# Kernel tuning notes

Hardware: AMD Instinct MI355X
Metric: run time of the kernel (lower is better)

The kernel has to match this reference:

```python
import jax, jax.numpy as jnp
import numpy as np

N_NODES = 100000
NINP = 128
N_EDGES = 1600000
EPS = 1e-12


def _gcn_conv(x, W, b, src, dst, deg_inv_sqrt):
    # PyG GCNConv: h = x W; out = D^{-1/2}(A+I)D^{-1/2} h + b
    h = x @ W  # [N, out_dim]
    norm = deg_inv_sqrt[src] * deg_inv_sqrt[dst]  # [E]
    agg = jax.ops.segment_sum(h[src] * norm[:, None], dst, num_segments=N_NODES)
    # self-loop contribution: weight deg_inv_sqrt[i]^2
    agg = agg + h * (deg_inv_sqrt ** 2)[:, None]
    return agg + b


def setup_inputs() -> dict:
    key = jax.random.key(0)
    k1, k2, k3, k4 = jax.random.split(key, 4)
    edge_index = jax.random.randint(k1, (2, N_EDGES), 0, N_NODES, dtype=jnp.int64)
    # embedding table (xavier-normal-like), padding_idx=0 row zeroed
    emb = jax.random.normal(k2, (N_NODES, NINP), dtype=jnp.float32) * (2.0 / (N_NODES + NINP)) ** 0.5
    emb = emb.at[0].set(0.0)
    W1 = jax.random.normal(k3, (NINP, 2 * NINP), dtype=jnp.float32) * (1.0 / NINP) ** 0.5
    b1 = jnp.zeros((2 * NINP,), dtype=jnp.float32)
    W2 = jax.random.normal(k4, (2 * NINP, NINP), dtype=jnp.float32) * (1.0 / (2 * NINP)) ** 0.5
    b2 = jnp.zeros((NINP,), dtype=jnp.float32)
    return {"emb": emb, "W1": W1, "b1": b1, "W2": W2, "b2": b2, "edge_index": edge_index}


def reference(emb, W1, b1, W2, b2, edge_index):
    src, dst = edge_index[0], edge_index[1]
    # symmetric GCN degree with self-loops (in-degree on dst + 1)
    deg = jax.ops.segment_sum(jnp.ones_like(dst, dtype=emb.dtype), dst, num_segments=N_NODES) + 1.0
    deg_inv_sqrt = jax.lax.rsqrt(deg)
    x = _gcn_conv(emb, W1, b1, src, dst, deg_inv_sqrt)  # [N, 2*ninp]
    # F.normalize(p=2, dim=-1)
    x = x / jnp.maximum(jnp.linalg.norm(x, axis=-1, keepdims=True), EPS)
    # dropout in eval mode (identity)
    out = _gcn_conv(x, W2, b2, src, dst, deg_inv_sqrt)  # [N, ninp]
    return out
```

## Files before the change

kernel.cpp:

```cpp
#include <hip/hip_runtime.h>
#include <hip/hip_bf16.h>

typedef __attribute__((ext_vector_type(8))) short bf16x8;
typedef __attribute__((ext_vector_type(4))) float f32x4;

#define NBUCK 391
#define BCAP 8192


__device__ __forceinline__ ushort f2bf(float f) {
    unsigned int b = __float_as_uint(f);
    unsigned int r = (b + 0x7fffu + ((b >> 16) & 1u)) >> 16;
    return (ushort)r;
}
__device__ __forceinline__ float bflo(uint v) { return __uint_as_float(v << 16); }
__device__ __forceinline__ float bfhi(uint v) { return __uint_as_float(v & 0xffff0000u); }


__global__ __launch_bounds__(256) void prep_kernel(const float* __restrict__ W1, ushort* __restrict__ W1t,
                                                   const float* __restrict__ W2, ushort* __restrict__ W2t,
                                                   int* __restrict__ gcur) {
    int b = blockIdx.x, t = threadIdx.x;
    if (b == 0) {
        if (t < NBUCK) gcur[t] = 0;
        if (t + 256 < NBUCK) gcur[t + 256] = 0;
    } else if (b <= 128) {
        int i = (b - 1) * 256 + t;
        int n = i >> 7, k = i & 127;
        W1t[i] = f2bf(W1[(size_t)k * 256 + n]);
    } else {
        int i = (b - 129) * 256 + t;
        int n = i >> 8, k = i & 255;
        W2t[i] = f2bf(W2[(size_t)k * 128 + n]);
    }
}


__global__ __launch_bounds__(256) void bucket_kernel(const int* __restrict__ src, const int* __restrict__ dst,
                                                     int* __restrict__ gcur, int2* __restrict__ pairs,
                                                     int E, int chunk) {
    __shared__ int lcnt[NBUCK];
    for (int t = threadIdx.x; t < NBUCK; t += 256) lcnt[t] = 0;
    __syncthreads();
    int e0 = blockIdx.x * chunk;
    int e1 = e0 + chunk; if (e1 > E) e1 = E;
    for (int e = e0 + (int)threadIdx.x; e < e1; e += 256)
        atomicAdd(&lcnt[dst[e] >> 8], 1);
    __syncthreads();
    for (int t = threadIdx.x; t < NBUCK; t += 256) {
        int c = lcnt[t];
        lcnt[t] = c ? atomicAdd(&gcur[t], c) : 0;
    }
    __syncthreads();
    for (int e = e0 + (int)threadIdx.x; e < e1; e += 256) {
        int d = dst[e], s = src[e];
        int b = d >> 8;
        int p = atomicAdd(&lcnt[b], 1);
        if (p < BCAP) pairs[(size_t)b * BCAP + p] = make_int2(d, s);
    }
}


__global__ __launch_bounds__(512) void scan_buckets(const int* __restrict__ gcur, int* __restrict__ bbase,
                                                    int* __restrict__ offs, int Nn, int E) {
    int i = threadIdx.x;
    int v = (i < NBUCK) ? min(gcur[i], BCAP) : 0;
    int lane = i & 63, wid = i >> 6;
    int x = v;
#pragma unroll
    for (int d = 1; d < 64; d <<= 1) {
        int y = __shfl_up(x, d, 64);
        if (lane >= d) x += y;
    }
    __shared__ int wsum[8], wpre[8];
    if (lane == 63) wsum[wid] = x;
    __syncthreads();
    if (i == 0) {
        int run = 0;
        for (int w = 0; w < 8; ++w) { wpre[w] = run; run += wsum[w]; }
        offs[Nn] = E;
    }
    __syncthreads();
    if (i < NBUCK) bbase[i] = x - v + wpre[wid];
}


__global__ __launch_bounds__(256) void csr_kernel(const int2* __restrict__ pairs, const int* __restrict__ gcur,
                                                  const int* __restrict__ bbase,
                                                  int* __restrict__ offs, float* __restrict__ dis,
                                                  int* __restrict__ csr, int Nn) {
    int b = blockIdx.x;
    int n0 = b << 8;
    int ne = min(gcur[b], BCAP);
    __shared__ int cnt[256], off[256], pos[256];
    int i = threadIdx.x;
    cnt[i] = 0;
    __syncthreads();
    const int2* pp = pairs + (size_t)b * BCAP;
    for (int e = i; e < ne; e += 256)
        atomicAdd(&cnt[pp[e].x - n0], 1);
    __syncthreads();
    int lane = i & 63, wid = i >> 6;
    int v = cnt[i];
    int x = v;
#pragma unroll
    for (int d = 1; d < 64; d <<= 1) {
        int y = __shfl_up(x, d, 64);
        if (lane >= d) x += y;
    }
    __shared__ int wsum[4], wpre[4];
    if (lane == 63) wsum[wid] = x;
    __syncthreads();
    if (i == 0) {
        int run = 0;
        for (int w = 0; w < 4; ++w) { wpre[w] = run; run += wsum[w]; }
    }
    __syncthreads();
    int excl = x - v + wpre[wid];
    off[i] = excl;
    pos[i] = 0;
    int n = n0 + i;
    if (n < Nn) {
        offs[n] = bbase[b] + excl;
        dis[n] = rsqrtf((float)v + 1.0f);
    }
    __syncthreads();
    int base = bbase[b];
    for (int e = i; e < ne; e += 256) {
        int2 r = pp[e];
        int li = r.x - n0;
        int p = atomicAdd(&pos[li], 1);
        csr[base + off[li] + p] = r.y;
    }
}


__global__ void cast_scale_kernel(const float4* __restrict__ in, const float* __restrict__ dis,
                                  ushort4* __restrict__ out, int n4) {
    int stride = gridDim.x * blockDim.x;
    for (int i = blockIdx.x * blockDim.x + threadIdx.x; i < n4; i += stride) {
        float s = dis[i >> 5];
        float4 v = in[i];
        ushort4 o;
        o.x = f2bf(v.x * s); o.y = f2bf(v.y * s); o.z = f2bf(v.z * s); o.w = f2bf(v.w * s);
        out[i] = o;
    }
}


template <bool BIAS, bool BF16OUT>
__global__ __launch_bounds__(256) void agg_kernel(const uint* __restrict__ tbl,
                                                  const int* __restrict__ offs,
                                                  const int* __restrict__ rec,
                                                  const float* __restrict__ dis,
                                                  const float* __restrict__ bias,
                                                  void* __restrict__ outp, int Nn) {
    int gw = (int)((blockIdx.x * 256 + threadIdx.x) >> 6);
    uint lane = threadIdx.x & 63;
    if (gw >= Nn) return;
    float dn = dis[gw];
    int e0 = offs[gw], e1 = offs[gw + 1];
    uint hv = tbl[(uint)gw * 64u + lane];
    float ax = bflo(hv), ay = bfhi(hv);

    for (int base = e0; base < e1; base += 16) {
        int ee = base + (int)(lane & 15u);
        uint rr = (uint)rec[ee < e1 ? ee : e1 - 1];
        uint vv[16];
#pragma unroll
        for (int j = 0; j < 16; ++j) {
            uint idx = (uint)__shfl((int)rr, j, 64);
            vv[j] = tbl[idx * 64u + lane];
        }
#pragma unroll
        for (int j = 0; j < 16; ++j) {
            uint v = (base + j < e1) ? vv[j] : 0u;
            ax += bflo(v);
            ay += bfhi(v);
        }
    }

    ax *= dn; ay *= dn;
    if (BIAS) {
        float2 bv = reinterpret_cast<const float2*>(bias)[lane];
        ax += bv.x; ay += bv.y;
    }
    if (BF16OUT) {
        reinterpret_cast<uint*>(outp)[(uint)gw * 64u + lane] =
            (uint)f2bf(ax) | ((uint)f2bf(ay) << 16);
    } else {
        float2 o; o.x = ax; o.y = ay;
        reinterpret_cast<float2*>(outp)[(uint)gw * 64u + lane] = o;
    }
}


__global__ __launch_bounds__(256) void fused_gemm(const ushort* __restrict__ A,
                                                  const ushort* __restrict__ W1t,
                                                  const float* __restrict__ bias1,
                                                  const ushort* __restrict__ W2t,
                                                  const float* __restrict__ dsc,
                                                  ushort* __restrict__ out2, int M, int NT) {
    __shared__ ushort xt[64 * 256];
    __shared__ float ssl[4][64];
    int lane = threadIdx.x & 63, wid = threadIdx.x >> 6;
    int g = lane >> 4;
    int i15 = lane & 15;
    int koff = g * 8;

    bf16x8 b1f[4][4];
#pragma unroll
    for (int ns = 0; ns < 4; ++ns) {
        int c = wid * 64 + ns * 16 + i15;
        const bf16x8* p = reinterpret_cast<const bf16x8*>(W1t + (size_t)c * 128 + koff);
#pragma unroll
        for (int ks = 0; ks < 4; ++ks) b1f[ns][ks] = p[ks * 4];
    }
    float bv[4];
#pragma unroll
    for (int ns = 0; ns < 4; ++ns) bv[ns] = bias1[wid * 64 + ns * 16 + i15];

    for (int t = blockIdx.x; t < NT; t += gridDim.x) {
        int m0 = t * 64;

        bf16x8 a[4][4];
#pragma unroll
        for (int ms = 0; ms < 4; ++ms) {
            int r = m0 + ms * 16 + i15;
            if (r >= M) r = M - 1;
            const bf16x8* p = reinterpret_cast<const bf16x8*>(A + (size_t)r * 128 + koff);
#pragma unroll
            for (int ks = 0; ks < 4; ++ks) a[ms][ks] = p[ks * 4];
        }

        f32x4 acc[4][4];
#pragma unroll
        for (int ms = 0; ms < 4; ++ms)
#pragma unroll
            for (int ns = 0; ns < 4; ++ns) acc[ms][ns] = (f32x4){0.f, 0.f, 0.f, 0.f};
#pragma unroll
        for (int ks = 0; ks < 4; ++ks)
#pragma unroll
            for (int ms = 0; ms < 4; ++ms)
#pragma unroll
                for (int ns = 0; ns < 4; ++ns)
                    acc[ms][ns] = __builtin_amdgcn_mfma_f32_16x16x32_bf16(a[ms][ks], b1f[ns][ks], acc[ms][ns], 0, 0, 0);

        bf16x8 b2f[2][8];
#pragma unroll
        for (int ns = 0; ns < 2; ++ns) {
            int c = wid * 32 + ns * 16 + i15;
            const bf16x8* p = reinterpret_cast<const bf16x8*>(W2t + (size_t)c * 256 + koff);
#pragma unroll
            for (int ks = 0; ks < 8; ++ks) b2f[ns][ks] = p[ks * 4];
        }

        float ps[4][4];
#pragma unroll
        for (int ms = 0; ms < 4; ++ms)
#pragma unroll
            for (int r = 0; r < 4; ++r) {
                float s = 0.f;
#pragma unroll
                for (int ns = 0; ns < 4; ++ns) {
                    float v = acc[ms][ns][r] + bv[ns];
                    acc[ms][ns][r] = v;
                    s += v * v;
                }
                ps[ms][r] = s;
            }
#pragma unroll
        for (int d = 1; d < 16; d <<= 1)
#pragma unroll
            for (int ms = 0; ms < 4; ++ms)
#pragma unroll
                for (int r = 0; r < 4; ++r) ps[ms][r] += __shfl_xor(ps[ms][r], d, 64);
        if (i15 == 0) {
#pragma unroll
            for (int ms = 0; ms < 4; ++ms)
#pragma unroll
                for (int r = 0; r < 4; ++r) ssl[wid][ms * 16 + g * 4 + r] = ps[ms][r];
        }
        __syncthreads();
#pragma unroll
        for (int ms = 0; ms < 4; ++ms)
#pragma unroll
            for (int r = 0; r < 4; ++r) {
                int rt = ms * 16 + g * 4 + r;
                float tot = ssl[0][rt] + ssl[1][rt] + ssl[2][rt] + ssl[3][rt];
                float inv = 1.0f / fmaxf(sqrtf(tot), 1e-12f);
                int sw = (rt & 7) << 3;
#pragma unroll
                for (int ns = 0; ns < 4; ++ns) {
                    int col = wid * 64 + ns * 16 + i15;
                    xt[(rt * 256 + col) ^ sw] = f2bf(acc[ms][ns][r] * inv);
                }
            }
        __syncthreads();

        f32x4 acc2[4][2];
#pragma unroll
        for (int ms = 0; ms < 4; ++ms)
#pragma unroll
            for (int ns = 0; ns < 2; ++ns) acc2[ms][ns] = (f32x4){0.f, 0.f, 0.f, 0.f};
#pragma unroll
        for (int ks = 0; ks < 8; ++ks) {
            bf16x8 a2[4];
#pragma unroll
            for (int ms = 0; ms < 4; ++ms) {
                int rowA = ms * 16 + i15;
                int eb = (rowA * 256 + koff + ks * 32) ^ ((rowA & 7) << 3);
                a2[ms] = *reinterpret_cast<const bf16x8*>(&xt[eb]);
            }
#pragma unroll
            for (int ms = 0; ms < 4; ++ms)
#pragma unroll
                for (int ns = 0; ns < 2; ++ns)
                    acc2[ms][ns] = __builtin_amdgcn_mfma_f32_16x16x32_bf16(a2[ms], b2f[ns][ks], acc2[ms][ns], 0, 0, 0);
        }
#pragma unroll
        for (int ms = 0; ms < 4; ++ms)
#pragma unroll
            for (int r = 0; r < 4; ++r) {
                int row = m0 + ms * 16 + g * 4 + r;
                if (row < M) {
                    float sc = dsc[row];
#pragma unroll
                    for (int ns = 0; ns < 2; ++ns)
                        out2[(size_t)row * 128 + wid * 32 + ns * 16 + i15] = f2bf(acc2[ms][ns][r] * sc);
                }
            }
        __syncthreads();
    }
}


extern "C" void kernel_launch(void* const* d_in, const int* in_sizes, int n_in,
                              void* d_out, int out_size, void* d_ws, size_t ws_size,
                              hipStream_t stream) {
    const float* emb = (const float*)d_in[0];
    const float* W1 = (const float*)d_in[1];
    const float* b1 = (const float*)d_in[2];
    const float* W2 = (const float*)d_in[3];
    const float* b2 = (const float*)d_in[4];
    const int* eidx = (const int*)d_in[5];

    const int Nn = in_sizes[0] / 128;
    const int E = in_sizes[5] / 2;
    const int* srcp = eidx;
    const int* dstp = eidx + E;

    float* ws = (float*)d_ws;
    size_t o = 0;
    uint* tbl1 = (uint*)(ws + o);  o += (size_t)Nn * 64;
    uint* axb = (uint*)(ws + o);   o += (size_t)Nn * 64;
    uint* tbl2 = (uint*)(ws + o);  o += (size_t)Nn * 64;
    ushort* W1t = (ushort*)(ws + o); o += 128 * 256 / 2;
    ushort* W2t = (ushort*)(ws + o); o += 256 * 128 / 2;
    float* dis = ws + o;    o += Nn;
    int* gcur = (int*)(ws + o);   o += NBUCK + 1;
    int* bbase = (int*)(ws + o);  o += NBUCK + 1;
    int* offs = (int*)(ws + o);   o += Nn + 16;
    int* csr = (int*)(ws + o);    o += E;
    int2* pairs = (int2*)(ws + o); o += (size_t)NBUCK * BCAP * 2;

    prep_kernel<<<257, 256, 0, stream>>>(W1, W1t, W2, W2t, gcur);

    int B1B = 512;
    int chunk = (E + B1B - 1) / B1B;
    bucket_kernel<<<B1B, 256, 0, stream>>>(srcp, dstp, gcur, pairs, E, chunk);
    scan_buckets<<<1, 512, 0, stream>>>(gcur, bbase, offs, Nn, E);
    csr_kernel<<<NBUCK, 256, 0, stream>>>(pairs, gcur, bbase, offs, dis, csr, Nn);

    int n4 = Nn * 128 / 4;
    cast_scale_kernel<<<2048, 256, 0, stream>>>((const float4*)emb, dis, (ushort4*)tbl1, n4);

    agg_kernel<false, true><<<(Nn + 3) / 4, 256, 0, stream>>>(tbl1, offs, csr, dis, nullptr, axb, Nn);
    int NT = (Nn + 63) / 64;
    fused_gemm<<<512, 256, 0, stream>>>((const ushort*)axb, W1t, b1, W2t, dis, (ushort*)tbl2, Nn, NT);

    agg_kernel<true, false><<<(Nn + 3) / 4, 256, 0, stream>>>(tbl2, offs, csr, dis, b2, d_out, Nn);
}
```

Before: 259.1 us.

## Restructure fused GEMM to one tile per 512-thread block with LDS-staged A

Replaces the persistent 512-block, 4-wave grid-stride loop with a one-tile-per-block launch of 8 waves, halving the per-wave column slice in both GEMMs. The A tile is loaded coalesced into swizzled shared memory instead of each wave reading rows directly from global memory, and launch bounds request higher occupancy. The aim is more parallelism, fewer registers per wave and better latency hiding in this stage. In exchange, weight fragments are reloaded for every tile instead of once per persistent block, LDS use per block grows, and the row-norm reduction now sums over 8 waves.

```diff
diff --git a/kernel.cpp b/kernel.cpp
--- a/kernel.cpp
+++ b/kernel.cpp
@@ -195,143 +195,149 @@
 }
 
 
-__global__ __launch_bounds__(256) void fused_gemm(const ushort* __restrict__ A,
-                                                  const ushort* __restrict__ W1t,
-                                                  const float* __restrict__ bias1,
-                                                  const ushort* __restrict__ W2t,
-                                                  const float* __restrict__ dsc,
-                                                  ushort* __restrict__ out2, int M, int NT) {
-    __shared__ ushort xt[64 * 256];
-    __shared__ float ssl[4][64];
-    int lane = threadIdx.x & 63, wid = threadIdx.x >> 6;
-    int g = lane >> 4;
-    int i15 = lane & 15;
+__global__ __launch_bounds__(512, 4) void fused_gemm(const ushort* __restrict__ A,
+                                                     const ushort* __restrict__ W1t,
+                                                     const float* __restrict__ bias1,
+                                                     const ushort* __restrict__ W2t,
+                                                     const float* __restrict__ dsc,
+                                                     ushort* __restrict__ out2, int M) {
+    __shared__ __align__(16) ushort sA[64 * 128];
+    __shared__ __align__(16) ushort xt[64 * 256];
+    __shared__ float ssl[8][64];
+    int tid = threadIdx.x;
+    int lane = tid & 63, wid = tid >> 6;
+    int g = lane >> 4, i15 = lane & 15;
     int koff = g * 8;
-
-    bf16x8 b1f[4][4];
-#pragma unroll
-    for (int ns = 0; ns < 4; ++ns) {
-        int c = wid * 64 + ns * 16 + i15;
+    int m0 = blockIdx.x * 64;
+
+    {
+        const char* Ab = reinterpret_cast<const char*>(A);
+        char* sAb = reinterpret_cast<char*>(sA);
+#pragma unroll
+        for (int j = 0; j < 2; ++j) {
+            int byte = j * 8192 + tid * 16;
+            int row = byte >> 8;
+            int grow = m0 + row; if (grow >= M) grow = M - 1;
+            bf16x8 v = *reinterpret_cast<const bf16x8*>(Ab + (size_t)grow * 256 + (byte & 255));
+            *reinterpret_cast<bf16x8*>(sAb + (byte ^ ((row & 7) << 4))) = v;
+        }
+    }
+
+    bf16x8 b1f[2][4];
+    float bv[2];
+#pragma unroll
+    for (int ns = 0; ns < 2; ++ns) {
+        int c = wid * 32 + ns * 16 + i15;
         const bf16x8* p = reinterpret_cast<const bf16x8*>(W1t + (size_t)c * 128 + koff);
 #pragma unroll
         for (int ks = 0; ks < 4; ++ks) b1f[ns][ks] = p[ks * 4];
-    }
-    float bv[4];
-#pragma unroll
-    for (int ns = 0; ns < 4; ++ns) bv[ns] = bias1[wid * 64 + ns * 16 + i15];
-
-    for (int t = blockIdx.x; t < NT; t += gridDim.x) {
-        int m0 = t * 64;
-
-        bf16x8 a[4][4];
+        bv[ns] = bias1[c];
+    }
+    __syncthreads();
+
+    const char* sAb = reinterpret_cast<const char*>(sA);
+    f32x4 acc[4][2];
+#pragma unroll
+    for (int ms = 0; ms < 4; ++ms)
+#pragma unroll
+        for (int ns = 0; ns < 2; ++ns) acc[ms][ns] = (f32x4){0.f, 0.f, 0.f, 0.f};
+#pragma unroll
+    for (int ks = 0; ks < 4; ++ks) {
+        bf16x8 a[4];
 #pragma unroll
         for (int ms = 0; ms < 4; ++ms) {
-            int r = m0 + ms * 16 + i15;
-            if (r >= M) r = M - 1;
-            const bf16x8* p = reinterpret_cast<const bf16x8*>(A + (size_t)r * 128 + koff);
-#pragma unroll
-            for (int ks = 0; ks < 4; ++ks) a[ms][ks] = p[ks * 4];
-        }
-
-        f32x4 acc[4][4];
+            int row = ms * 16 + i15;
+            int byte = row * 256 + ks * 64 + g * 16;
+            a[ms] = *reinterpret_cast<const bf16x8*>(sAb + (byte ^ ((row & 7) << 4)));
+        }
 #pragma unroll
         for (int ms = 0; ms < 4; ++ms)
 #pragma unroll
-            for (int ns = 0; ns < 4; ++ns) acc[ms][ns] = (f32x4){0.f, 0.f, 0.f, 0.f};
-#pragma unroll
-        for (int ks = 0; ks < 4; ++ks)
-#pragma unroll
-            for (int ms = 0; ms < 4; ++ms)
-#pragma unroll
-                for (int ns = 0; ns < 4; ++ns)
-                    acc[ms][ns] = __builtin_amdgcn_mfma_f32_16x16x32_bf16(a[ms][ks], b1f[ns][ks], acc[ms][ns], 0, 0, 0);
-
-        bf16x8 b2f[2][8];
-#pragma unroll
-        for (int ns = 0; ns < 2; ++ns) {
-            int c = wid * 32 + ns * 16 + i15;
-            const bf16x8* p = reinterpret_cast<const bf16x8*>(W2t + (size_t)c * 256 + koff);
-#pragma unroll
-            for (int ks = 0; ks < 8; ++ks) b2f[ns][ks] = p[ks * 4];
-        }
-
-        float ps[4][4];
+            for (int ns = 0; ns < 2; ++ns)
+                acc[ms][ns] = __builtin_amdgcn_mfma_f32_16x16x32_bf16(a[ms], b1f[ns][ks], acc[ms][ns], 0, 0, 0);
+    }
+
+    float ps[4][4];
+#pragma unroll
+    for (int ms = 0; ms < 4; ++ms)
+#pragma unroll
+        for (int r = 0; r < 4; ++r) {
+            float s = 0.f;
+#pragma unroll
+            for (int ns = 0; ns < 2; ++ns) {
+                float v = acc[ms][ns][r] + bv[ns];
+                acc[ms][ns][r] = v;
+                s += v * v;
+            }
+            ps[ms][r] = s;
+        }
+#pragma unroll
+    for (int d = 1; d < 16; d <<= 1)
 #pragma unroll
         for (int ms = 0; ms < 4; ++ms)
 #pragma unroll
-            for (int r = 0; r < 4; ++r) {
-                float s = 0.f;
-#pragma unroll
-                for (int ns = 0; ns < 4; ++ns) {
-                    float v = acc[ms][ns][r] + bv[ns];
-                    acc[ms][ns][r] = v;
-                    s += v * v;
-                }
-                ps[ms][r] = s;
+            for (int r = 0; r < 4; ++r) ps[ms][r] += __shfl_xor(ps[ms][r], d, 64);
+    if (i15 == 0) {
+#pragma unroll
+        for (int ms = 0; ms < 4; ++ms)
+#pragma unroll
+            for (int r = 0; r < 4; ++r) ssl[wid][ms * 16 + g * 4 + r] = ps[ms][r];
+    }
+    __syncthreads();
+
+#pragma unroll
+    for (int ms = 0; ms < 4; ++ms)
+#pragma unroll
+        for (int r = 0; r < 4; ++r) {
+            int rt = ms * 16 + g * 4 + r;
+            float tot = 0.f;
+#pragma unroll
+            for (int w = 0; w < 8; ++w) tot += ssl[w][rt];
+            float inv = 1.0f / fmaxf(sqrtf(tot), 1e-12f);
+            int sw = (rt & 7) << 3;
+#pragma unroll
+            for (int ns = 0; ns < 2; ++ns) {
+                int col = wid * 32 + ns * 16 + i15;
+                xt[(rt * 256 + col) ^ sw] = f2bf(acc[ms][ns][r] * inv);
             }
-#pragma unroll
-        for (int d = 1; d < 16; d <<= 1)
-#pragma unroll
-            for (int ms = 0; ms < 4; ++ms)
-#pragma unroll
-                for (int r = 0; r < 4; ++r) ps[ms][r] += __shfl_xor(ps[ms][r], d, 64);
-        if (i15 == 0) {
-#pragma unroll
-            for (int ms = 0; ms < 4; ++ms)
-#pragma unroll
-                for (int r = 0; r < 4; ++r) ssl[wid][ms * 16 + g * 4 + r] = ps[ms][r];
-        }
-        __syncthreads();
+        }
+    __syncthreads();
+
+    bf16x8 b2f[8];
+    {
+        int c = wid * 16 + i15;
+        const bf16x8* p = reinterpret_cast<const bf16x8*>(W2t + (size_t)c * 256 + koff);
+#pragma unroll
+        for (int ks = 0; ks < 8; ++ks) b2f[ks] = p[ks * 4];
+    }
+
+    f32x4 acc2[4];
+#pragma unroll
+    for (int ms = 0; ms < 4; ++ms) acc2[ms] = (f32x4){0.f, 0.f, 0.f, 0.f};
+#pragma unroll
+    for (int ks = 0; ks < 8; ++ks) {
+        bf16x8 a2[4];
+#pragma unroll
+        for (int ms = 0; ms < 4; ++ms) {
+            int rowA = ms * 16 + i15;
+            int eb = (rowA * 256 + koff + ks * 32) ^ ((rowA & 7) << 3);
+            a2[ms] = *reinterpret_cast<const bf16x8*>(&xt[eb]);
+        }
 #pragma unroll
         for (int ms = 0; ms < 4; ++ms)
-#pragma unroll
-            for (int r = 0; r < 4; ++r) {
-                int rt = ms * 16 + g * 4 + r;
-                float tot = ssl[0][rt] + ssl[1][rt] + ssl[2][rt] + ssl[3][rt];
-                float inv = 1.0f / fmaxf(sqrtf(tot), 1e-12f);
-                int sw = (rt & 7) << 3;
-#pragma unroll
-                for (int ns = 0; ns < 4; ++ns) {
-                    int col = wid * 64 + ns * 16 + i15;
-                    xt[(rt * 256 + col) ^ sw] = f2bf(acc[ms][ns][r] * inv);
-                }
+            acc2[ms] = __builtin_amdgcn_mfma_f32_16x16x32_bf16(a2[ms], b2f[ks], acc2[ms], 0, 0, 0);
+    }
+
+#pragma unroll
+    for (int ms = 0; ms < 4; ++ms)
+#pragma unroll
+        for (int r = 0; r < 4; ++r) {
+            int row = m0 + ms * 16 + g * 4 + r;
+            if (row < M) {
+                float sc = dsc[row];
+                out2[(size_t)row * 128 + wid * 16 + i15] = f2bf(acc2[ms][r] * sc);
             }
-        __syncthreads();
-
-        f32x4 acc2[4][2];
-#pragma unroll
-        for (int ms = 0; ms < 4; ++ms)
-#pragma unroll
-            for (int ns = 0; ns < 2; ++ns) acc2[ms][ns] = (f32x4){0.f, 0.f, 0.f, 0.f};
-#pragma unroll
-        for (int ks = 0; ks < 8; ++ks) {
-            bf16x8 a2[4];
-#pragma unroll
-            for (int ms = 0; ms < 4; ++ms) {
-                int rowA = ms * 16 + i15;
-                int eb = (rowA * 256 + koff + ks * 32) ^ ((rowA & 7) << 3);
-                a2[ms] = *reinterpret_cast<const bf16x8*>(&xt[eb]);
-            }
-#pragma unroll
-            for (int ms = 0; ms < 4; ++ms)
-#pragma unroll
-                for (int ns = 0; ns < 2; ++ns)
-                    acc2[ms][ns] = __builtin_amdgcn_mfma_f32_16x16x32_bf16(a2[ms], b2f[ns][ks], acc2[ms][ns], 0, 0, 0);
-        }
-#pragma unroll
-        for (int ms = 0; ms < 4; ++ms)
-#pragma unroll
-            for (int r = 0; r < 4; ++r) {
-                int row = m0 + ms * 16 + g * 4 + r;
-                if (row < M) {
-                    float sc = dsc[row];
-#pragma unroll
-                    for (int ns = 0; ns < 2; ++ns)
-                        out2[(size_t)row * 128 + wid * 32 + ns * 16 + i15] = f2bf(acc2[ms][ns][r] * sc);
-                }
-            }
-        __syncthreads();
-    }
+        }
 }
 
 
@@ -376,8 +382,7 @@
     cast_scale_kernel<<<2048, 256, 0, stream>>>((const float4*)emb, dis, (ushort4*)tbl1, n4);
 
     agg_kernel<false, true><<<(Nn + 3) / 4, 256, 0, stream>>>(tbl1, offs, csr, dis, nullptr, axb, Nn);
-    int NT = (Nn + 63) / 64;
-    fused_gemm<<<512, 256, 0, stream>>>((const ushort*)axb, W1t, b1, W2t, dis, (ushort*)tbl2, Nn, NT);
+    fused_gemm<<<(Nn + 63) / 64, 512, 0, stream>>>((const ushort*)axb, W1t, b1, W2t, dis, (ushort*)tbl2, Nn);
 
     agg_kernel<true, false><<<(Nn + 3) / 4, 256, 0, stream>>>(tbl2, offs, csr, dis, b2, d_out, Nn);
 }
```

Result: faster. 234.7 us (-9.4%).
